# Performance work log

Measured on AMD Instinct MI355X. Metric: run time of the kernel, lower is better.

Reference implementation:

```python
import jax, jax.numpy as jnp
import numpy as np

EMBED_SIZE = 1024

def setup_inputs() -> dict:
    key = jax.random.key(0)
    k1, k2, k3, k4 = jax.random.split(key, 4)
    B, T, C, H = 8, 2048, 1024, 128
    embeddings = jax.random.normal(k1, (B, T, C), dtype=jnp.float32)
    # nn.Linear(embed, head, bias=False) weight applied as x @ W^T; store as [C, H] for x @ W
    scale = 1.0 / np.sqrt(C)
    Wq = jax.random.normal(k2, (C, H), dtype=jnp.float32) * scale
    Wk = jax.random.normal(k3, (C, H), dtype=jnp.float32) * scale
    Wv = jax.random.normal(k4, (C, H), dtype=jnp.float32) * scale
    return {"embeddings": embeddings, "Wq": Wq, "Wk": Wk, "Wv": Wv}

def reference(embeddings, Wq, Wk, Wv):
    B, T, C = embeddings.shape
    q = jnp.einsum('btc,ch->bth', embeddings, Wq)
    k = jnp.einsum('btc,ch->bth', embeddings, Wk)
    v = jnp.einsum('btc,ch->bth', embeddings, Wv)
    # NOTE: source scales by embed_size**-0.5 (not head_size**-0.5)
    wei = jnp.einsum('bqh,bkh->bqk', q, k) * (C ** -0.5)
    causal = jnp.tril(jnp.ones((T, T), dtype=bool))  # tril buffer
    wei = jnp.where(causal, wei, -jnp.inf)
    wei = jax.nn.softmax(wei, axis=-1)
    return jnp.einsum('bqk,bkh->bqh', wei, v)
```

## Files before the change

### kernel.cpp

```cpp
#include <hip/hip_runtime.h>
#include <hip/hip_bf16.h>

typedef __bf16 bf16x8 __attribute__((ext_vector_type(8)));
typedef float f32x4 __attribute__((ext_vector_type(4)));
typedef ushort us8 __attribute__((ext_vector_type(8)));

#define MFMA(a, b, c) __builtin_amdgcn_mfma_f32_16x16x32_bf16((a), (b), (c), 0, 0, 0)

static constexpr int T_LEN = 2048;
static constexpr int C_DIM = 1024;
static constexpr int H_DIM = 128;
static constexpr int M_ROWS = 8 * 2048;
static constexpr int N_COLS = 384;
static constexpr int SLOTS_PER_B = 528;
static constexpr int PSTR = 72;
static constexpr int KSTR = 136;
static constexpr int VSTR = 72;
static constexpr int BSTR = 40;

__device__ __forceinline__ ushort f2bf(float f) {
  union { float f; unsigned u; } v; v.f = f;
  unsigned u = v.u;
  u += 0x7fffu + ((u >> 16) & 1u);
  return (ushort)(u >> 16);
}
__device__ __forceinline__ float bf2f(ushort u) {
  union { unsigned u; float f; } v; v.u = (unsigned)u << 16;
  return v.f;
}

__global__ void wt_convert(const float* __restrict__ Wq,
                           const float* __restrict__ Wk,
                           const float* __restrict__ Wv,
                           ushort* __restrict__ wt) {
  int o = blockIdx.x * 256 + threadIdx.x;
  int kt = o / 12288;
  int rem = o - kt * 12288;
  int gc = rem >> 5;
  int kk = rem & 31;
  int c  = kt * 32 + kk;
  int mat = gc >> 7;
  int h   = gc & 127;
  const float* W = (mat == 0) ? Wq : ((mat == 1) ? Wk : Wv);
  wt[o] = f2bf(W[c * H_DIM + h]);
}

__global__ __launch_bounds__(256, 4) void qkv_gemm(const float* __restrict__ X,
                                                   const ushort* __restrict__ wt,
                                                   ushort* __restrict__ qws,
                                                   ushort* __restrict__ kws,
                                                   ushort* __restrict__ vtws) {
  __shared__ ushort As[2][32 * BSTR];
  __shared__ ushort Bs[2][192 * BSTR];
  const int tid = threadIdx.x;
  const int wid = tid >> 6, lane = tid & 63;
  const int lg = lane >> 4, lr = lane & 15;
  const int m0 = (blockIdx.x >> 1) * 32;
  const int n0 = (blockIdx.x & 1) * 192;
  const float QSCL = 0.03125f * 1.44269504f;

  const int ar = tid >> 3, ac = tid & 7;
  const float* gA = &X[(size_t)(m0 + ar) * C_DIM + ac * 4];

  const int u0 = tid * 24;
  const int br0 = u0 >> 5,        bk0 = u0 & 31;
  const int br1 = (u0 + 8) >> 5,  bk1 = (u0 + 8) & 31;
  const int br2 = (u0 + 16) >> 5, bk2 = (u0 + 16) & 31;

  f32x4 acc[2][3];
#pragma unroll
  for (int r = 0; r < 2; ++r)
#pragma unroll
    for (int c = 0; c < 3; ++c)
      acc[r][c] = f32x4{0.f, 0.f, 0.f, 0.f};

  float4 areg = *(const float4*)gA;
  const ushort* gB0 = &wt[(size_t)(0 * 384 + n0) * 32 + u0];
  us8 breg0 = *(const us8*)(gB0);
  us8 breg1 = *(const us8*)(gB0 + 8);
  us8 breg2 = *(const us8*)(gB0 + 16);

  for (int kt = 0; kt < 32; ++kt) {
    const int cur = kt & 1;
    __syncthreads();
    {
      ushort4 av;
      av.x = f2bf(areg.x); av.y = f2bf(areg.y);
      av.z = f2bf(areg.z); av.w = f2bf(areg.w);
      *(ushort4*)&As[cur][ar * BSTR + ac * 4] = av;
      *(us8*)&Bs[cur][br0 * BSTR + bk0] = breg0;
      *(us8*)&Bs[cur][br1 * BSTR + bk1] = breg1;
      *(us8*)&Bs[cur][br2 * BSTR + bk2] = breg2;
    }
    if (kt + 1 < 32) {
      areg = *(const float4*)(gA + (kt + 1) * 32);
      const ushort* gB = &wt[(size_t)((kt + 1) * 384 + n0) * 32 + u0];
      breg0 = *(const us8*)(gB);
      breg1 = *(const us8*)(gB + 8);
      breg2 = *(const us8*)(gB + 16);
    }
    __syncthreads();

    bf16x8 a0 = *(const bf16x8*)&As[cur][(lr) * BSTR + lg * 8];
    bf16x8 a1 = *(const bf16x8*)&As[cur][(16 + lr) * BSTR + lg * 8];
#pragma unroll
    for (int c = 0; c < 3; ++c) {
      bf16x8 bf = *(const bf16x8*)&Bs[cur][(wid * 48 + c * 16 + lr) * BSTR + lg * 8];
      acc[0][c] = MFMA(a0, bf, acc[0][c]);
      acc[1][c] = MFMA(a1, bf, acc[1][c]);
    }
  }

#pragma unroll
  for (int c = 0; c < 3; ++c) {
    int gc = n0 + wid * 48 + c * 16 + lr;
    int mat = gc >> 7, h = gc & 127;
#pragma unroll
    for (int r = 0; r < 2; ++r) {
#pragma unroll
      for (int j = 0; j < 4; ++j) {
        int gr = m0 + r * 16 + lg * 4 + j;
        float val = acc[r][c][j];
        ushort ov = f2bf(mat == 0 ? val * QSCL : val);
        if (mat == 0) {
          qws[(size_t)gr * H_DIM + h] = ov;
        } else if (mat == 1) {
          kws[(size_t)gr * H_DIM + h] = ov;
        } else {
          int b = gr >> 11, t = gr & 2047;
          vtws[((size_t)b * H_DIM + h) * T_LEN + t] = ov;
        }
      }
    }
  }
}

__global__ __launch_bounds__(256, 3) void attn_part(const ushort* __restrict__ qws,
                                                    const ushort* __restrict__ kws,
                                                    const ushort* __restrict__ vtws,
                                                    float* __restrict__ pml,
                                                    ushort* __restrict__ pacc,
                                                    float* __restrict__ out) {
  __shared__ ushort Klds[64 * KSTR];
  __shared__ ushort Vlds[128 * VSTR];
  __shared__ ushort Pw[4][16 * PSTR];

  const int tid = threadIdx.x;
  const int wid = tid >> 6, lane = tid & 63;
  const int lg = lane >> 4, lr = lane & 15;
  const int bid = blockIdx.x;
  const int b = bid & 7;
  const int item = bid >> 3;

  int qb, ck;
  bool direct;
  if (item < 8) {
    qb = item; ck = 0; direct = true;
  } else {
    const int p = item - 8;
    direct = false;
    if (p < 12)      { int q = p / 3;        qb = 8 + q;  ck = p - q * 3; }
    else if (p < 28) { int q = (p - 12) >> 2; qb = 12 + q; ck = (p - 12) & 3; }
    else if (p < 48) { int q = (p - 28) / 5; qb = 16 + q; ck = (p - 28) - q * 5; }
    else if (p < 72) { int q = (p - 48) / 6; qb = 20 + q; ck = (p - 48) - q * 6; }
    else if (p < 100){ int q = (p - 72) / 7; qb = 24 + q; ck = (p - 72) - q * 7; }
    else             { int q = (p - 100) >> 3; qb = 28 + q; ck = (p - 100) & 7; }
  }
  const int qi = qb * 4 + wid;
  const int q0 = qi * 16;
  const int nt = qb + 1;
  const int kvt_lo = direct ? 0 : ck * 4;
  const int kvt_hi = direct ? nt : min(ck * 4 + 4, nt);
  const size_t tokbase = (size_t)b * T_LEN;
  const ushort* vb = vtws + (size_t)b * H_DIM * T_LEN;

  const int kr = tid >> 2, kseg = tid & 3;
  const int vr = tid >> 1, vseg = tid & 1;
  const ushort* gK = &kws[(tokbase + kr) * H_DIM + kseg * 32];
  const ushort* gV = &vb[(size_t)vr * T_LEN + vseg * 32];

  bf16x8 qf[4];
#pragma unroll
  for (int hk = 0; hk < 4; ++hk)
    qf[hk] = *(const bf16x8*)&qws[(tokbase + q0 + lr) * H_DIM + hk * 32 + lg * 8];

  f32x4 acc[8];
#pragma unroll
  for (int hf = 0; hf < 8; ++hf) acc[hf] = f32x4{0.f, 0.f, 0.f, 0.f};
  float mrun = -INFINITY, lrun = 0.f;

  ushort* Pme = &Pw[wid][0];

  us8 kreg[4], vreg[4];
#pragma unroll
  for (int i = 0; i < 4; ++i) {
    kreg[i] = *(const us8*)(gK + (size_t)kvt_lo * 64 * H_DIM + i * 8);
    vreg[i] = *(const us8*)(gV + kvt_lo * 64 + i * 8);
  }

  for (int kvt = kvt_lo; kvt < kvt_hi; ++kvt) {
    const int kv0 = kvt * 64;

    __syncthreads();
#pragma unroll
    for (int i = 0; i < 4; ++i) {
      *(us8*)&Klds[kr * KSTR + kseg * 32 + i * 8] = kreg[i];
      *(us8*)&Vlds[vr * VSTR + vseg * 32 + i * 8] = vreg[i];
    }
    if (kvt + 1 < kvt_hi) {
#pragma unroll
      for (int i = 0; i < 4; ++i) {
        kreg[i] = *(const us8*)(gK + (size_t)(kv0 + 64) * H_DIM + i * 8);
        vreg[i] = *(const us8*)(gV + kv0 + 64 + i * 8);
      }
    }
    __syncthreads();

    f32x4 s[4];
#pragma unroll
    for (int c = 0; c < 4; ++c) {
      f32x4 sc = f32x4{0.f, 0.f, 0.f, 0.f};
#pragma unroll
      for (int hk = 0; hk < 4; ++hk) {
        bf16x8 kf = *(const bf16x8*)&Klds[(c * 16 + lr) * KSTR + hk * 32 + lg * 8];
        sc = MFMA(kf, qf[hk], sc);
      }
      s[c] = sc;
    }

    if (kvt == nt - 1) {
#pragma unroll
      for (int c = 0; c < 4; ++c)
#pragma unroll
        for (int j = 0; j < 4; ++j) {
          int kv = kv0 + c * 16 + lg * 4 + j;
          if (kv > q0 + lr) s[c][j] = -INFINITY;
        }
    }

    float mx = s[0][0];
#pragma unroll
    for (int c = 0; c < 4; ++c)
#pragma unroll
      for (int j = 0; j < 4; ++j) mx = fmaxf(mx, s[c][j]);
    mx = fmaxf(mx, __shfl_xor(mx, 16));
    mx = fmaxf(mx, __shfl_xor(mx, 32));

    float mnew = fmaxf(mrun, mx);
    float scold = exp2f(mrun - mnew);

    float rsum = 0.f;
#pragma unroll
    for (int c = 0; c < 4; ++c)
#pragma unroll
      for (int j = 0; j < 4; ++j) {
        float p = exp2f(s[c][j] - mnew);
        s[c][j] = p;
        rsum += p;
      }

#pragma unroll
    for (int c = 0; c < 4; ++c) {
      ushort4 u;
      u.x = f2bf(s[c][0]); u.y = f2bf(s[c][1]);
      u.z = f2bf(s[c][2]); u.w = f2bf(s[c][3]);
      *(ushort4*)&Pme[lr * PSTR + c * 16 + lg * 4] = u;
    }

    bf16x8 v0[8];
#pragma unroll
    for (int hf = 0; hf < 8; ++hf)
      v0[hf] = *(const bf16x8*)&Vlds[(hf * 16 + lr) * VSTR + lg * 8];

    rsum += __shfl_xor(rsum, 16);
    rsum += __shfl_xor(rsum, 32);

    lrun = lrun * scold + rsum;
    mrun = mnew;
#pragma unroll
    for (int hf = 0; hf < 8; ++hf)
#pragma unroll
      for (int j = 0; j < 4; ++j) acc[hf][j] *= scold;

    bf16x8 pa0 = *(const bf16x8*)&Pme[lr * PSTR + lg * 8];
    bf16x8 pa1 = *(const bf16x8*)&Pme[lr * PSTR + 32 + lg * 8];

#pragma unroll
    for (int hf = 0; hf < 8; ++hf)
      acc[hf] = MFMA(v0[hf], pa0, acc[hf]);
#pragma unroll
    for (int hf = 0; hf < 8; ++hf) {
      bf16x8 v1 = *(const bf16x8*)&Vlds[(hf * 16 + lr) * VSTR + 32 + lg * 8];
      acc[hf] = MFMA(v1, pa1, acc[hf]);
    }
  }

  if (direct) {
    float inv = 1.0f / lrun;
    float* op = &out[(tokbase + q0 + lr) * H_DIM + lg * 4];
#pragma unroll
    for (int hf = 0; hf < 8; ++hf) {
      float4 r0 = make_float4(acc[hf][0] * inv, acc[hf][1] * inv,
                              acc[hf][2] * inv, acc[hf][3] * inv);
      *(float4*)(op + hf * 16) = r0;
    }
  } else {
    int base;
    if (qi < 48)       base = (qi - 32) * 3;
    else if (qi < 64)  base = 48 + (qi - 48) * 4;
    else if (qi < 80)  base = 112 + (qi - 64) * 5;
    else if (qi < 96)  base = 192 + (qi - 80) * 6;
    else if (qi < 112) base = 288 + (qi - 96) * 7;
    else               base = 400 + (qi - 112) * 8;
    const size_t slot = (size_t)b * SLOTS_PER_B + base + ck;
    if (lg == 0) {
      pml[slot * 32 + lr] = mrun;
      pml[slot * 32 + 16 + lr] = lrun;
    }
    ushort* ap = &pacc[slot * 2048 + (size_t)lr * 128 + lg * 4];
#pragma unroll
    for (int hf = 0; hf < 8; ++hf) {
      ushort4 u;
      u.x = f2bf(acc[hf][0]); u.y = f2bf(acc[hf][1]);
      u.z = f2bf(acc[hf][2]); u.w = f2bf(acc[hf][3]);
      *(ushort4*)(ap + hf * 16) = u;
    }
  }
}

__global__ __launch_bounds__(256) void attn_merge(const float* __restrict__ pml,
                                                  const ushort* __restrict__ pacc,
                                                  float* __restrict__ out) {
  const int bid = blockIdx.x;
  const int b = bid & 7, qi = (bid >> 3) + 32;
  int base, nch;
  if (qi < 48)       { base = (qi - 32) * 3;        nch = 3; }
  else if (qi < 64)  { base = 48 + (qi - 48) * 4;   nch = 4; }
  else if (qi < 80)  { base = 112 + (qi - 64) * 5;  nch = 5; }
  else if (qi < 96)  { base = 192 + (qi - 80) * 6;  nch = 6; }
  else if (qi < 112) { base = 288 + (qi - 96) * 7;  nch = 7; }
  else               { base = 400 + (qi - 112) * 8; nch = 8; }
  const size_t slot0 = (size_t)b * SLOTS_PER_B + base;
  const int tid = threadIdx.x;
  const int r = tid >> 4, c0 = (tid & 15) * 8;

  float mrun = -INFINITY, L = 0.f;
  float o[8];
#pragma unroll
  for (int i = 0; i < 8; ++i) o[i] = 0.f;

  for (int ck = 0; ck < nch; ++ck) {
    const size_t s = slot0 + ck;
    float m = pml[s * 32 + r];
    float l = pml[s * 32 + 16 + r];
    float mn = fmaxf(mrun, m);
    float sc = exp2f(mrun - mn);
    float w  = exp2f(m - mn);
    L = L * sc + w * l;
    const ushort* ap = &pacc[s * 2048 + (size_t)r * 128 + c0];
    ushort4 u0 = *(const ushort4*)ap;
    ushort4 u1 = *(const ushort4*)(ap + 4);
    o[0] = o[0] * sc + w * bf2f(u0.x); o[1] = o[1] * sc + w * bf2f(u0.y);
    o[2] = o[2] * sc + w * bf2f(u0.z); o[3] = o[3] * sc + w * bf2f(u0.w);
    o[4] = o[4] * sc + w * bf2f(u1.x); o[5] = o[5] * sc + w * bf2f(u1.y);
    o[6] = o[6] * sc + w * bf2f(u1.z); o[7] = o[7] * sc + w * bf2f(u1.w);
    mrun = mn;
  }
  float invL = 1.0f / L;
  float4 r0 = make_float4(o[0] * invL, o[1] * invL, o[2] * invL, o[3] * invL);
  float4 r1 = make_float4(o[4] * invL, o[5] * invL, o[6] * invL, o[7] * invL);
  float* op = &out[((size_t)b * T_LEN + qi * 16 + r) * H_DIM + c0];
  *(float4*)op = r0;
  *(float4*)(op + 4) = r1;
}

extern "C" void kernel_launch(void* const* d_in, const int* in_sizes, int n_in,
                              void* d_out, int out_size, void* d_ws, size_t ws_size,
                              hipStream_t stream) {
  const float* emb = (const float*)d_in[0];
  const float* Wq  = (const float*)d_in[1];
  const float* Wk  = (const float*)d_in[2];
  const float* Wv  = (const float*)d_in[3];
  float* out = (float*)d_out;

  ushort* wt   = (ushort*)d_ws;
  ushort* qws  = wt  + (size_t)N_COLS * C_DIM;
  ushort* kws  = qws + (size_t)M_ROWS * H_DIM;
  ushort* vtws = kws + (size_t)M_ROWS * H_DIM;
  ushort* pacc = vtws + (size_t)8 * H_DIM * T_LEN;
  float*  pml  = (float*)d_ws;

  wt_convert<<<(N_COLS * C_DIM) / 256, 256, 0, stream>>>(Wq, Wk, Wv, wt);
  qkv_gemm<<<(M_ROWS / 32) * 2, 256, 0, stream>>>(emb, wt, qws, kws, vtws);
  attn_part<<<8 * 140, 256, 0, stream>>>(qws, kws, vtws, pml, pacc, out);
  attn_merge<<<8 * 96, 256, 0, stream>>>(pml, pacc, out);
}
```

Baseline: 80.80 us.

## Enlarge QKV GEMM M-tile with swizzled LDS and two-deep register prefetch

The QKV projection GEMM now processes 64 rows per block instead of 32, so each B fragment read from LDS feeds four MFMAs instead of two, and half as many blocks reload the weight tile. The padded LDS rows are replaced by an XOR-swizzled layout. The single-buffer loop is replaced by a two-iteration unrolled loop that keeps two K-tiles prefetched in registers and uses a lightweight lgkmcnt wait plus barrier. The cost is more registers and accumulators (launch bounds reduced to 2 blocks per SM) and fewer blocks in the grid.

```diff
diff --git a/kernel.cpp b/kernel.cpp
--- a/kernel.cpp
+++ b/kernel.cpp
@@ -16,7 +16,6 @@
 static constexpr int PSTR = 72;
 static constexpr int KSTR = 136;
 static constexpr int VSTR = 72;
-static constexpr int BSTR = 40;
 
 __device__ __forceinline__ ushort f2bf(float f) {
   union { float f; unsigned u; } v; v.f = f;
@@ -27,6 +26,16 @@
 __device__ __forceinline__ float bf2f(ushort u) {
   union { unsigned u; float f; } v; v.u = (unsigned)u << 16;
   return v.f;
+}
+
+__device__ __forceinline__ void waitbar() {
+  asm volatile("s_waitcnt lgkmcnt(0)" ::: "memory");
+  __builtin_amdgcn_s_barrier();
+  __builtin_amdgcn_sched_barrier(0);
+}
+
+__device__ __forceinline__ int swz_byte(int row, int slot) {
+  return (row >> 1) * 128 + (row & 1) * 64 + ((slot * 16) ^ (((row >> 1) & 3) << 4));
 }
 
 __global__ void wt_convert(const float* __restrict__ Wq,
@@ -45,70 +54,138 @@
   wt[o] = f2bf(W[c * H_DIM + h]);
 }
 
-__global__ __launch_bounds__(256, 4) void qkv_gemm(const float* __restrict__ X,
+__global__ __launch_bounds__(256, 2) void qkv_gemm(const float* __restrict__ X,
                                                    const ushort* __restrict__ wt,
                                                    ushort* __restrict__ qws,
                                                    ushort* __restrict__ kws,
                                                    ushort* __restrict__ vtws) {
-  __shared__ ushort As[2][32 * BSTR];
-  __shared__ ushort Bs[2][192 * BSTR];
+  __shared__ ushort As[2][32 * 64];
+  __shared__ ushort Bs[2][96 * 64];
   const int tid = threadIdx.x;
   const int wid = tid >> 6, lane = tid & 63;
   const int lg = lane >> 4, lr = lane & 15;
-  const int m0 = (blockIdx.x >> 1) * 32;
+  const int m0 = (blockIdx.x >> 1) * 64;
   const int n0 = (blockIdx.x & 1) * 192;
   const float QSCL = 0.03125f * 1.44269504f;
 
-  const int ar = tid >> 3, ac = tid & 7;
-  const float* gA = &X[(size_t)(m0 + ar) * C_DIM + ac * 4];
-
-  const int u0 = tid * 24;
-  const int br0 = u0 >> 5,        bk0 = u0 & 31;
-  const int br1 = (u0 + 8) >> 5,  bk1 = (u0 + 8) & 31;
-  const int br2 = (u0 + 16) >> 5, bk2 = (u0 + 16) & 31;
-
-  f32x4 acc[2][3];
-#pragma unroll
-  for (int r = 0; r < 2; ++r)
+  const int ar = tid >> 2, ac = tid & 3;
+  const float* gA = &X[(size_t)(m0 + ar) * C_DIM + ac * 8];
+  const int awb = swz_byte(ar, ac);
+
+  const int bwb0 = swz_byte((tid) >> 2, (tid) & 3);
+  const int bwb1 = swz_byte((tid + 256) >> 2, (tid + 256) & 3);
+  const int bwb2 = swz_byte((tid + 512) >> 2, (tid + 512) & 3);
+
+  const int afb = swz_byte(lr, lg);
+  const int bfb = swz_byte(wid * 48 + lr, lg);
+
+  f32x4 acc[4][3];
+#pragma unroll
+  for (int r = 0; r < 4; ++r)
 #pragma unroll
     for (int c = 0; c < 3; ++c)
       acc[r][c] = f32x4{0.f, 0.f, 0.f, 0.f};
 
-  float4 areg = *(const float4*)gA;
-  const ushort* gB0 = &wt[(size_t)(0 * 384 + n0) * 32 + u0];
-  us8 breg0 = *(const us8*)(gB0);
-  us8 breg1 = *(const us8*)(gB0 + 8);
-  us8 breg2 = *(const us8*)(gB0 + 16);
-
-  for (int kt = 0; kt < 32; ++kt) {
-    const int cur = kt & 1;
-    __syncthreads();
+  float4 aE0, aE1, aO0, aO1;
+  us8 bE0, bE1, bE2, bO0, bO1, bO2;
+
+  {
+    float4 x0 = *(const float4*)gA;
+    float4 x1 = *(const float4*)(gA + 4);
+    const ushort* gB = &wt[(size_t)n0 * 32];
+    us8 b0 = *(const us8*)(gB + (size_t)tid * 8);
+    us8 b1 = *(const us8*)(gB + (size_t)(tid + 256) * 8);
+    us8 b2 = *(const us8*)(gB + (size_t)(tid + 512) * 8);
+    us8 av;
+    av[0] = f2bf(x0.x); av[1] = f2bf(x0.y); av[2] = f2bf(x0.z); av[3] = f2bf(x0.w);
+    av[4] = f2bf(x1.x); av[5] = f2bf(x1.y); av[6] = f2bf(x1.z); av[7] = f2bf(x1.w);
+    *(us8*)((char*)&As[0][0] + awb) = av;
+    *(us8*)((char*)&Bs[0][0] + bwb0) = b0;
+    *(us8*)((char*)&Bs[0][0] + bwb1) = b1;
+    *(us8*)((char*)&Bs[0][0] + bwb2) = b2;
+  }
+  {
+    aE0 = *(const float4*)(gA + 32);
+    aE1 = *(const float4*)(gA + 36);
+    const ushort* gB = &wt[(size_t)(384 + n0) * 32];
+    bE0 = *(const us8*)(gB + (size_t)tid * 8);
+    bE1 = *(const us8*)(gB + (size_t)(tid + 256) * 8);
+    bE2 = *(const us8*)(gB + (size_t)(tid + 512) * 8);
+    aO0 = *(const float4*)(gA + 64);
+    aO1 = *(const float4*)(gA + 68);
+    const ushort* gB2 = &wt[(size_t)(2 * 384 + n0) * 32];
+    bO0 = *(const us8*)(gB2 + (size_t)tid * 8);
+    bO1 = *(const us8*)(gB2 + (size_t)(tid + 256) * 8);
+    bO2 = *(const us8*)(gB2 + (size_t)(tid + 512) * 8);
+  }
+  waitbar();
+
+  for (int k2 = 0; k2 < 32; k2 += 2) {
     {
-      ushort4 av;
-      av.x = f2bf(areg.x); av.y = f2bf(areg.y);
-      av.z = f2bf(areg.z); av.w = f2bf(areg.w);
-      *(ushort4*)&As[cur][ar * BSTR + ac * 4] = av;
-      *(us8*)&Bs[cur][br0 * BSTR + bk0] = breg0;
-      *(us8*)&Bs[cur][br1 * BSTR + bk1] = breg1;
-      *(us8*)&Bs[cur][br2 * BSTR + bk2] = breg2;
-    }
-    if (kt + 1 < 32) {
-      areg = *(const float4*)(gA + (kt + 1) * 32);
-      const ushort* gB = &wt[(size_t)((kt + 1) * 384 + n0) * 32 + u0];
-      breg0 = *(const us8*)(gB);
-      breg1 = *(const us8*)(gB + 8);
-      breg2 = *(const us8*)(gB + 16);
-    }
-    __syncthreads();
-
-    bf16x8 a0 = *(const bf16x8*)&As[cur][(lr) * BSTR + lg * 8];
-    bf16x8 a1 = *(const bf16x8*)&As[cur][(16 + lr) * BSTR + lg * 8];
-#pragma unroll
-    for (int c = 0; c < 3; ++c) {
-      bf16x8 bf = *(const bf16x8*)&Bs[cur][(wid * 48 + c * 16 + lr) * BSTR + lg * 8];
-      acc[0][c] = MFMA(a0, bf, acc[0][c]);
-      acc[1][c] = MFMA(a1, bf, acc[1][c]);
-    }
+      us8 av;
+      av[0] = f2bf(aE0.x); av[1] = f2bf(aE0.y); av[2] = f2bf(aE0.z); av[3] = f2bf(aE0.w);
+      av[4] = f2bf(aE1.x); av[5] = f2bf(aE1.y); av[6] = f2bf(aE1.z); av[7] = f2bf(aE1.w);
+      *(us8*)((char*)&As[1][0] + awb) = av;
+      *(us8*)((char*)&Bs[1][0] + bwb0) = bE0;
+      *(us8*)((char*)&Bs[1][0] + bwb1) = bE1;
+      *(us8*)((char*)&Bs[1][0] + bwb2) = bE2;
+    }
+    if (k2 + 3 < 32) {
+      aE0 = *(const float4*)(gA + (k2 + 3) * 32);
+      aE1 = *(const float4*)(gA + (k2 + 3) * 32 + 4);
+      const ushort* gB = &wt[(size_t)((k2 + 3) * 384 + n0) * 32];
+      bE0 = *(const us8*)(gB + (size_t)tid * 8);
+      bE1 = *(const us8*)(gB + (size_t)(tid + 256) * 8);
+      bE2 = *(const us8*)(gB + (size_t)(tid + 512) * 8);
+    }
+    {
+      bf16x8 a0 = *(const bf16x8*)((const char*)&As[0][0] + afb);
+      bf16x8 a1 = *(const bf16x8*)((const char*)&As[0][0] + afb + 1024);
+      bf16x8 a2 = *(const bf16x8*)((const char*)&As[0][0] + afb + 2048);
+      bf16x8 a3 = *(const bf16x8*)((const char*)&As[0][0] + afb + 3072);
+#pragma unroll
+      for (int c = 0; c < 3; ++c) {
+        bf16x8 bf = *(const bf16x8*)((const char*)&Bs[0][0] + bfb + c * 1024);
+        acc[0][c] = MFMA(a0, bf, acc[0][c]);
+        acc[1][c] = MFMA(a1, bf, acc[1][c]);
+        acc[2][c] = MFMA(a2, bf, acc[2][c]);
+        acc[3][c] = MFMA(a3, bf, acc[3][c]);
+      }
+    }
+    waitbar();
+
+    if (k2 + 2 < 32) {
+      us8 av;
+      av[0] = f2bf(aO0.x); av[1] = f2bf(aO0.y); av[2] = f2bf(aO0.z); av[3] = f2bf(aO0.w);
+      av[4] = f2bf(aO1.x); av[5] = f2bf(aO1.y); av[6] = f2bf(aO1.z); av[7] = f2bf(aO1.w);
+      *(us8*)((char*)&As[0][0] + awb) = av;
+      *(us8*)((char*)&Bs[0][0] + bwb0) = bO0;
+      *(us8*)((char*)&Bs[0][0] + bwb1) = bO1;
+      *(us8*)((char*)&Bs[0][0] + bwb2) = bO2;
+    }
+    if (k2 + 4 < 32) {
+      aO0 = *(const float4*)(gA + (k2 + 4) * 32);
+      aO1 = *(const float4*)(gA + (k2 + 4) * 32 + 4);
+      const ushort* gB = &wt[(size_t)((k2 + 4) * 384 + n0) * 32];
+      bO0 = *(const us8*)(gB + (size_t)tid * 8);
+      bO1 = *(const us8*)(gB + (size_t)(tid + 256) * 8);
+      bO2 = *(const us8*)(gB + (size_t)(tid + 512) * 8);
+    }
+    {
+      bf16x8 a0 = *(const bf16x8*)((const char*)&As[1][0] + afb);
+      bf16x8 a1 = *(const bf16x8*)((const char*)&As[1][0] + afb + 1024);
+      bf16x8 a2 = *(const bf16x8*)((const char*)&As[1][0] + afb + 2048);
+      bf16x8 a3 = *(const bf16x8*)((const char*)&As[1][0] + afb + 3072);
+#pragma unroll
+      for (int c = 0; c < 3; ++c) {
+        bf16x8 bf = *(const bf16x8*)((const char*)&Bs[1][0] + bfb + c * 1024);
+        acc[0][c] = MFMA(a0, bf, acc[0][c]);
+        acc[1][c] = MFMA(a1, bf, acc[1][c]);
+        acc[2][c] = MFMA(a2, bf, acc[2][c]);
+        acc[3][c] = MFMA(a3, bf, acc[3][c]);
+      }
+    }
+    waitbar();
   }
 
 #pragma unroll
@@ -116,7 +193,7 @@
     int gc = n0 + wid * 48 + c * 16 + lr;
     int mat = gc >> 7, h = gc & 127;
 #pragma unroll
-    for (int r = 0; r < 2; ++r) {
+    for (int r = 0; r < 4; ++r) {
 #pragma unroll
       for (int j = 0; j < 4; ++j) {
         int gr = m0 + r * 16 + lg * 4 + j;
@@ -391,7 +468,7 @@
   float*  pml  = (float*)d_ws;
 
   wt_convert<<<(N_COLS * C_DIM) / 256, 256, 0, stream>>>(Wq, Wk, Wv, wt);
-  qkv_gemm<<<(M_ROWS / 32) * 2, 256, 0, stream>>>(emb, wt, qws, kws, vtws);
+  qkv_gemm<<<(M_ROWS / 64) * 2, 256, 0, stream>>>(emb, wt, qws, kws, vtws);
   attn_part<<<8 * 140, 256, 0, stream>>>(qws, kws, vtws, pml, pacc, out);
   attn_merge<<<8 * 96, 256, 0, stream>>>(pml, pacc, out);
 }
```

New measurement: 72.75 us. 1.11x faster.

## Preswizzle weights into MFMA fragment order and load B directly to registers

Applied to the files above, without the earlier changes.

The weight-conversion kernel now writes the bf16 weights in per-lane MFMA fragment order, so the QKV GEMM loads its B operands straight from global memory into registers and no longer stages them in shared memory. The A tile goes into an XOR-swizzled LDS layout with a single barrier per k-step (a custom waitcnt plus s_barrier), and the loop is unrolled by two with ping-pong register prefetch. This cuts LDS traffic and synchronisation in the projection GEMM, at the cost of more registers and each wave fetching its own B fragments from global/L2.

```diff
diff --git a/kernel.cpp b/kernel.cpp
--- a/kernel.cpp
+++ b/kernel.cpp
@@ -16,7 +16,6 @@
 static constexpr int PSTR = 72;
 static constexpr int KSTR = 136;
 static constexpr int VSTR = 72;
-static constexpr int BSTR = 40;
 
 __device__ __forceinline__ ushort f2bf(float f) {
   union { float f; unsigned u; } v; v.f = f;
@@ -27,6 +26,16 @@
 __device__ __forceinline__ float bf2f(ushort u) {
   union { unsigned u; float f; } v; v.u = (unsigned)u << 16;
   return v.f;
+}
+
+__device__ __forceinline__ void waitbar() {
+  asm volatile("s_waitcnt lgkmcnt(0)" ::: "memory");
+  __builtin_amdgcn_s_barrier();
+  __builtin_amdgcn_sched_barrier(0);
+}
+
+__device__ __forceinline__ int swz_byte(int row, int slot) {
+  return (row >> 1) * 128 + (row & 1) * 64 + ((slot * 16) ^ (((row >> 1) & 3) << 4));
 }
 
 __global__ void wt_convert(const float* __restrict__ Wq,
@@ -36,9 +45,11 @@
   int o = blockIdx.x * 256 + threadIdx.x;
   int kt = o / 12288;
   int rem = o - kt * 12288;
-  int gc = rem >> 5;
-  int kk = rem & 31;
-  int c  = kt * 32 + kk;
+  int cg = rem >> 9;
+  int lane = (rem >> 3) & 63;
+  int j = rem & 7;
+  int gc = cg * 16 + (lane & 15);
+  int c  = kt * 32 + (lane >> 4) * 8 + j;
   int mat = gc >> 7;
   int h   = gc & 127;
   const float* W = (mat == 0) ? Wq : ((mat == 1) ? Wk : Wv);
@@ -50,22 +61,20 @@
                                                    ushort* __restrict__ qws,
                                                    ushort* __restrict__ kws,
                                                    ushort* __restrict__ vtws) {
-  __shared__ ushort As[2][32 * BSTR];
-  __shared__ ushort Bs[2][192 * BSTR];
+  __shared__ ushort As[2][16 * 64];
   const int tid = threadIdx.x;
   const int wid = tid >> 6, lane = tid & 63;
   const int lg = lane >> 4, lr = lane & 15;
   const int m0 = (blockIdx.x >> 1) * 32;
   const int n0 = (blockIdx.x & 1) * 192;
+  const int cgb = (blockIdx.x & 1) * 12 + wid * 3;
   const float QSCL = 0.03125f * 1.44269504f;
 
   const int ar = tid >> 3, ac = tid & 7;
   const float* gA = &X[(size_t)(m0 + ar) * C_DIM + ac * 4];
-
-  const int u0 = tid * 24;
-  const int br0 = u0 >> 5,        bk0 = u0 & 31;
-  const int br1 = (u0 + 8) >> 5,  bk1 = (u0 + 8) & 31;
-  const int br2 = (u0 + 16) >> 5, bk2 = (u0 + 16) & 31;
+  const int awb = swz_byte(ar, ac >> 1) + (ac & 1) * 8;
+
+  const int afb = swz_byte(lr, lg);
 
   f32x4 acc[2][3];
 #pragma unroll
@@ -74,41 +83,77 @@
     for (int c = 0; c < 3; ++c)
       acc[r][c] = f32x4{0.f, 0.f, 0.f, 0.f};
 
-  float4 areg = *(const float4*)gA;
-  const ushort* gB0 = &wt[(size_t)(0 * 384 + n0) * 32 + u0];
-  us8 breg0 = *(const us8*)(gB0);
-  us8 breg1 = *(const us8*)(gB0 + 8);
-  us8 breg2 = *(const us8*)(gB0 + 16);
-
-  for (int kt = 0; kt < 32; ++kt) {
-    const int cur = kt & 1;
-    __syncthreads();
+  float4 aE, aO;
+  us8 bE0, bE1, bE2, bO0, bO1, bO2;
+
+  {
+    float4 x0 = *(const float4*)gA;
+    ushort4 av;
+    av.x = f2bf(x0.x); av.y = f2bf(x0.y); av.z = f2bf(x0.z); av.w = f2bf(x0.w);
+    *(ushort4*)((char*)&As[0][0] + awb) = av;
+  }
+  aE = *(const float4*)(gA + 32);
+  aO = *(const float4*)(gA + 64);
+  {
+    const ushort* g0 = &wt[((size_t)(0 * 24 + cgb) * 64 + lane) * 8];
+    bE0 = *(const us8*)(g0);
+    bE1 = *(const us8*)(g0 + 512);
+    bE2 = *(const us8*)(g0 + 1024);
+    const ushort* g1 = &wt[((size_t)(1 * 24 + cgb) * 64 + lane) * 8];
+    bO0 = *(const us8*)(g1);
+    bO1 = *(const us8*)(g1 + 512);
+    bO2 = *(const us8*)(g1 + 1024);
+  }
+  waitbar();
+
+  for (int k2 = 0; k2 < 32; k2 += 2) {
     {
       ushort4 av;
-      av.x = f2bf(areg.x); av.y = f2bf(areg.y);
-      av.z = f2bf(areg.z); av.w = f2bf(areg.w);
-      *(ushort4*)&As[cur][ar * BSTR + ac * 4] = av;
-      *(us8*)&Bs[cur][br0 * BSTR + bk0] = breg0;
-      *(us8*)&Bs[cur][br1 * BSTR + bk1] = breg1;
-      *(us8*)&Bs[cur][br2 * BSTR + bk2] = breg2;
-    }
-    if (kt + 1 < 32) {
-      areg = *(const float4*)(gA + (kt + 1) * 32);
-      const ushort* gB = &wt[(size_t)((kt + 1) * 384 + n0) * 32 + u0];
-      breg0 = *(const us8*)(gB);
-      breg1 = *(const us8*)(gB + 8);
-      breg2 = *(const us8*)(gB + 16);
-    }
-    __syncthreads();
-
-    bf16x8 a0 = *(const bf16x8*)&As[cur][(lr) * BSTR + lg * 8];
-    bf16x8 a1 = *(const bf16x8*)&As[cur][(16 + lr) * BSTR + lg * 8];
-#pragma unroll
-    for (int c = 0; c < 3; ++c) {
-      bf16x8 bf = *(const bf16x8*)&Bs[cur][(wid * 48 + c * 16 + lr) * BSTR + lg * 8];
-      acc[0][c] = MFMA(a0, bf, acc[0][c]);
-      acc[1][c] = MFMA(a1, bf, acc[1][c]);
-    }
+      av.x = f2bf(aE.x); av.y = f2bf(aE.y); av.z = f2bf(aE.z); av.w = f2bf(aE.w);
+      *(ushort4*)((char*)&As[1][0] + awb) = av;
+    }
+    if (k2 + 3 < 32) aE = *(const float4*)(gA + (k2 + 3) * 32);
+    {
+      bf16x8 a0 = *(const bf16x8*)((const char*)&As[0][0] + afb);
+      bf16x8 a1 = *(const bf16x8*)((const char*)&As[0][0] + afb + 1024);
+      acc[0][0] = MFMA(a0, (bf16x8)bE0, acc[0][0]);
+      acc[1][0] = MFMA(a1, (bf16x8)bE0, acc[1][0]);
+      acc[0][1] = MFMA(a0, (bf16x8)bE1, acc[0][1]);
+      acc[1][1] = MFMA(a1, (bf16x8)bE1, acc[1][1]);
+      acc[0][2] = MFMA(a0, (bf16x8)bE2, acc[0][2]);
+      acc[1][2] = MFMA(a1, (bf16x8)bE2, acc[1][2]);
+    }
+    if (k2 + 2 < 32) {
+      const ushort* g = &wt[((size_t)((k2 + 2) * 24 + cgb) * 64 + lane) * 8];
+      bE0 = *(const us8*)(g);
+      bE1 = *(const us8*)(g + 512);
+      bE2 = *(const us8*)(g + 1024);
+    }
+    waitbar();
+
+    if (k2 + 2 < 32) {
+      ushort4 av;
+      av.x = f2bf(aO.x); av.y = f2bf(aO.y); av.z = f2bf(aO.z); av.w = f2bf(aO.w);
+      *(ushort4*)((char*)&As[0][0] + awb) = av;
+    }
+    if (k2 + 4 < 32) aO = *(const float4*)(gA + (k2 + 4) * 32);
+    {
+      bf16x8 a0 = *(const bf16x8*)((const char*)&As[1][0] + afb);
+      bf16x8 a1 = *(const bf16x8*)((const char*)&As[1][0] + afb + 1024);
+      acc[0][0] = MFMA(a0, (bf16x8)bO0, acc[0][0]);
+      acc[1][0] = MFMA(a1, (bf16x8)bO0, acc[1][0]);
+      acc[0][1] = MFMA(a0, (bf16x8)bO1, acc[0][1]);
+      acc[1][1] = MFMA(a1, (bf16x8)bO1, acc[1][1]);
+      acc[0][2] = MFMA(a0, (bf16x8)bO2, acc[0][2]);
+      acc[1][2] = MFMA(a1, (bf16x8)bO2, acc[1][2]);
+    }
+    if (k2 + 3 < 32) {
+      const ushort* g = &wt[((size_t)((k2 + 3) * 24 + cgb) * 64 + lane) * 8];
+      bO0 = *(const us8*)(g);
+      bO1 = *(const us8*)(g + 512);
+      bO2 = *(const us8*)(g + 1024);
+    }
+    waitbar();
   }
 
 #pragma unroll
```

Result: faster. 78.36 us (-3.0%).

## Load QKV weight tiles directly into LDS in MFMA fragment order

Applied to the files above, without the earlier changes.

Reorders the pre-converted bf16 weight buffer so each 16-column group is stored in MFMA B-fragment lane order. The GEMM then streams weight tiles straight from global memory into LDS with global_load_lds, skipping the round-trip through registers. The k-loop is restructured so the next tile is prefetched while the current one is computed, with one barrier per iteration instead of two, and padding is dropped from the LDS tiles. The cost is reliance on correct ordering of async LDS writes around the barrier, and unpadded A-tile reads that may hit bank conflicts.

```diff
diff --git a/kernel.cpp b/kernel.cpp
--- a/kernel.cpp
+++ b/kernel.cpp
@@ -16,7 +16,6 @@
 static constexpr int PSTR = 72;
 static constexpr int KSTR = 136;
 static constexpr int VSTR = 72;
-static constexpr int BSTR = 40;
 
 __device__ __forceinline__ ushort f2bf(float f) {
   union { float f; unsigned u; } v; v.f = f;
@@ -27,6 +26,12 @@
 __device__ __forceinline__ float bf2f(ushort u) {
   union { unsigned u; float f; } v; v.u = (unsigned)u << 16;
   return v.f;
+}
+
+__device__ __forceinline__ void gl2lds16(const ushort* g, ushort* l) {
+  __builtin_amdgcn_global_load_lds(
+      (const __attribute__((address_space(1))) unsigned int*)(const void*)g,
+      (__attribute__((address_space(3))) unsigned int*)(void*)l, 16, 0, 0);
 }
 
 __global__ void wt_convert(const float* __restrict__ Wq,
@@ -36,9 +41,11 @@
   int o = blockIdx.x * 256 + threadIdx.x;
   int kt = o / 12288;
   int rem = o - kt * 12288;
-  int gc = rem >> 5;
-  int kk = rem & 31;
-  int c  = kt * 32 + kk;
+  int cg = rem >> 9;
+  int lane = (rem >> 3) & 63;
+  int j = rem & 7;
+  int gc = cg * 16 + (lane & 15);
+  int c  = kt * 32 + (lane >> 4) * 8 + j;
   int mat = gc >> 7;
   int h   = gc & 127;
   const float* W = (mat == 0) ? Wq : ((mat == 1) ? Wk : Wv);
@@ -50,8 +57,8 @@
                                                    ushort* __restrict__ qws,
                                                    ushort* __restrict__ kws,
                                                    ushort* __restrict__ vtws) {
-  __shared__ ushort As[2][32 * BSTR];
-  __shared__ ushort Bs[2][192 * BSTR];
+  __shared__ ushort As[2][32 * 32];
+  __shared__ ushort Bs[2][12 * 512];
   const int tid = threadIdx.x;
   const int wid = tid >> 6, lane = tid & 63;
   const int lg = lane >> 4, lr = lane & 15;
@@ -59,13 +66,13 @@
   const int n0 = (blockIdx.x & 1) * 192;
   const float QSCL = 0.03125f * 1.44269504f;
 
-  const int ar = tid >> 3, ac = tid & 7;
-  const float* gA = &X[(size_t)(m0 + ar) * C_DIM + ac * 4];
-
-  const int u0 = tid * 24;
-  const int br0 = u0 >> 5,        bk0 = u0 & 31;
-  const int br1 = (u0 + 8) >> 5,  bk1 = (u0 + 8) & 31;
-  const int br2 = (u0 + 16) >> 5, bk2 = (u0 + 16) & 31;
+  const int arow = tid >> 3;
+  const float* gA = &X[(size_t)(m0 + arow) * C_DIM + (tid & 7) * 4];
+  const int aws = arow * 32 + (tid & 7) * 4;
+
+  const size_t wtb0 = (size_t)((blockIdx.x & 1) * 12) * 512 + (size_t)wid * 512 + (size_t)lane * 8;
+
+  const int afb = lr * 32 + lg * 8;
 
   f32x4 acc[2][3];
 #pragma unroll
@@ -74,41 +81,45 @@
     for (int c = 0; c < 3; ++c)
       acc[r][c] = f32x4{0.f, 0.f, 0.f, 0.f};
 
-  float4 areg = *(const float4*)gA;
-  const ushort* gB0 = &wt[(size_t)(0 * 384 + n0) * 32 + u0];
-  us8 breg0 = *(const us8*)(gB0);
-  us8 breg1 = *(const us8*)(gB0 + 8);
-  us8 breg2 = *(const us8*)(gB0 + 16);
-
+  {
+    float4 x = *(const float4*)gA;
+    ushort4 av;
+    av.x = f2bf(x.x); av.y = f2bf(x.y); av.z = f2bf(x.z); av.w = f2bf(x.w);
+    *(ushort4*)&As[0][aws] = av;
+    const ushort* gB = wt + wtb0;
+    gl2lds16(gB,        &Bs[0][(size_t)wid * 512]);
+    gl2lds16(gB + 2048, &Bs[0][(size_t)(4 + wid) * 512]);
+    gl2lds16(gB + 4096, &Bs[0][(size_t)(8 + wid) * 512]);
+  }
+  __syncthreads();
+
+  int cur = 0;
   for (int kt = 0; kt < 32; ++kt) {
-    const int cur = kt & 1;
-    __syncthreads();
-    {
-      ushort4 av;
-      av.x = f2bf(areg.x); av.y = f2bf(areg.y);
-      av.z = f2bf(areg.z); av.w = f2bf(areg.w);
-      *(ushort4*)&As[cur][ar * BSTR + ac * 4] = av;
-      *(us8*)&Bs[cur][br0 * BSTR + bk0] = breg0;
-      *(us8*)&Bs[cur][br1 * BSTR + bk1] = breg1;
-      *(us8*)&Bs[cur][br2 * BSTR + bk2] = breg2;
-    }
+    float4 an;
     if (kt + 1 < 32) {
-      areg = *(const float4*)(gA + (kt + 1) * 32);
-      const ushort* gB = &wt[(size_t)((kt + 1) * 384 + n0) * 32 + u0];
-      breg0 = *(const us8*)(gB);
-      breg1 = *(const us8*)(gB + 8);
-      breg2 = *(const us8*)(gB + 16);
-    }
-    __syncthreads();
-
-    bf16x8 a0 = *(const bf16x8*)&As[cur][(lr) * BSTR + lg * 8];
-    bf16x8 a1 = *(const bf16x8*)&As[cur][(16 + lr) * BSTR + lg * 8];
+      an = *(const float4*)(gA + (kt + 1) * 32);
+      const ushort* gBn = wt + (size_t)(kt + 1) * 12288 + wtb0;
+      gl2lds16(gBn,        &Bs[cur ^ 1][(size_t)wid * 512]);
+      gl2lds16(gBn + 2048, &Bs[cur ^ 1][(size_t)(4 + wid) * 512]);
+      gl2lds16(gBn + 4096, &Bs[cur ^ 1][(size_t)(8 + wid) * 512]);
+    }
+
+    bf16x8 a0 = *(const bf16x8*)&As[cur][afb];
+    bf16x8 a1 = *(const bf16x8*)&As[cur][afb + 512];
 #pragma unroll
     for (int c = 0; c < 3; ++c) {
-      bf16x8 bf = *(const bf16x8*)&Bs[cur][(wid * 48 + c * 16 + lr) * BSTR + lg * 8];
+      bf16x8 bf = *(const bf16x8*)&Bs[cur][(size_t)(wid * 3 + c) * 512 + (size_t)lane * 8];
       acc[0][c] = MFMA(a0, bf, acc[0][c]);
       acc[1][c] = MFMA(a1, bf, acc[1][c]);
     }
+
+    if (kt + 1 < 32) {
+      ushort4 av;
+      av.x = f2bf(an.x); av.y = f2bf(an.y); av.z = f2bf(an.z); av.w = f2bf(an.w);
+      *(ushort4*)&As[cur ^ 1][aws] = av;
+    }
+    __syncthreads();
+    cur ^= 1;
   }
 
 #pragma unroll
```

Result: slower. 89.75 us (+11.1%).
